# Kernel optimization log

Hardware: AMD Instinct MI355X
Metric: run time of the kernel (lower is better)

## Reference

```python
import jax, jax.numpy as jnp
from jax import lax
import numpy as np

B, COND_C = 16, 256
IN_C, OUT_C, K = 64, 64, 3
H = W = 128
N_PARAM = K * K * IN_C * OUT_C + OUT_C  # 36928


def setup_inputs() -> dict:
    key = jax.random.key(0)
    k1, k2, k3, k4 = jax.random.split(key, 4)
    x = jax.random.normal(k1, (B, IN_C, H, W), dtype=jnp.float32)
    conditioning = jax.random.normal(k2, (B, COND_C), dtype=jnp.float32)
    # nn.Linear(cond_c, n_param): weight [n_param, cond_c], bias [n_param]
    W_cond = jax.random.normal(k3, (N_PARAM, COND_C), dtype=jnp.float32) * 0.02
    b_cond = jax.random.normal(k4, (N_PARAM,), dtype=jnp.float32) * 0.02
    return {"x": x, "conditioning": conditioning, "W_cond": W_cond, "b_cond": b_cond}


def reference(x, conditioning, W_cond, b_cond):
    # Hypernetwork: Linear + tanh*5 (ConditionerActivation)
    w_b = jnp.tanh(conditioning @ W_cond.T + b_cond) * 5.0  # [B, N_PARAM]
    bias = w_b[:, -OUT_C:]                                   # [B, out_c]
    w = w_b[:, :-OUT_C].reshape(B, OUT_C, IN_C, K, K)        # per-sample OIHW

    def conv_one(xi, wi, bi):
        # xi: [in_c, H, W], wi: [out_c, in_c, K, K], bi: [out_c]
        y = lax.conv_general_dilated(
            xi[None], wi,
            window_strides=(1, 1),
            padding=[(1, 1), (1, 1)],
            dimension_numbers=("NCHW", "OIHW", "NCHW"),
        )[0]
        return y + bi[:, None, None]

    return jax.vmap(conv_one)(x, w, bias)  # [B, out_c, H, W]
```

## Files before the change

### kernel.cpp

```cpp
#include <hip/hip_runtime.h>
#include <math.h>
#include <stdint.h>

#define B_    16
#define CONDC 256
#define ICn   64
#define OCn   64
#define Hn    128
#define Wn    128
#define NW    36864
#define NPARAM 36928

typedef _Float16 half8 __attribute__((ext_vector_type(8)));
typedef _Float16 half4 __attribute__((ext_vector_type(4)));
typedef float f32x4 __attribute__((ext_vector_type(4)));
typedef float f32x16 __attribute__((ext_vector_type(16)));

__device__ inline unsigned pk2(float a, float b) {
    union { _Float16 h[2]; unsigned u; } q;
    q.h[0] = (_Float16)a; q.h[1] = (_Float16)b;
    return q.u;
}

__global__ void transpose_k(const float* __restrict__ x, _Float16* __restrict__ xt) {
    __shared__ unsigned ls[4160];
    const int tid = threadIdx.x;
    const int bx  = blockIdx.x;

    if (bx < 2048) {
        const int b = bx >> 7, y = bx & 127;
        const float* xrow = x + (size_t)b * 1048576 + (size_t)y * 128;

        float4 va[4], vb[4];
        #pragma unroll
        for (int t = 0; t < 4; ++t) {
            int u = t * 256 + tid;
            int icp = u >> 5, xg = u & 31;
            const float* r0 = xrow + (size_t)(2 * icp) * 16384;
            va[t] = *((const float4*)r0 + xg);
            vb[t] = *((const float4*)(r0 + 16384) + xg);
        }
        __builtin_amdgcn_sched_barrier(0);

        #pragma unroll
        for (int t = 0; t < 4; ++t) {
            int u = t * 256 + tid;
            int icp = u >> 5, xg = u & 31;
            unsigned* dst = ls + icp * 130 + 4 * xg;
            *(uint2*)(dst)     = make_uint2(pk2(va[t].x, vb[t].x), pk2(va[t].y, vb[t].y));
            *(uint2*)(dst + 2) = make_uint2(pk2(va[t].z, vb[t].z), pk2(va[t].w, vb[t].w));
        }
        __syncthreads();

        _Float16* rowhalf = xt + (size_t)(b * 130 + y + 1) * 8320;
        #pragma unroll
        for (int t = 0; t < 5; ++t) {
            int u = t * 256 + tid;
            if (u < 1040) {
                int xp = u >> 3, g = u & 7;
                uint4 val = make_uint4(0u, 0u, 0u, 0u);
                if (xp > 0 && xp < 129) {
                    int xx = xp - 1;
                    val.x = ls[(4 * g + 0) * 130 + xx];
                    val.y = ls[(4 * g + 1) * 130 + xx];
                    val.z = ls[(4 * g + 2) * 130 + xx];
                    val.w = ls[(4 * g + 3) * 130 + xx];
                }
                *(uint4*)(rowhalf + (size_t)u * 8) = val;
            }
        }
    } else {
        const int q = bx - 2048;
        const int b = q >> 1, yp = (q & 1) ? 129 : 0;
        _Float16* rowhalf = xt + (size_t)(b * 130 + yp) * 8320;
        uint4 z = make_uint4(0u, 0u, 0u, 0u);
        for (int u = tid; u < 1040; u += 256)
            *(uint4*)(rowhalf + (size_t)u * 8) = z;
    }
}

__global__ __launch_bounds__(256, 4) void gemm_k(const float* __restrict__ cond,
                                                 const float* __restrict__ Wc,
                                                 const float* __restrict__ bc,
                                                 _Float16* __restrict__ wt,
                                                 float* __restrict__ bias) {
    __shared__ _Float16 wl[64 * 280];
    const int tid = threadIdx.x;
    const int pbase = blockIdx.x * 64;

    float4 v[16];
    #pragma unroll
    for (int t = 0; t < 16; ++t) {
        int u = t * 256 + tid;
        int pl = u >> 6, kg = u & 63;
        v[t] = *((const float4*)(Wc + (size_t)(pbase + pl) * 256) + kg);
    }
    __builtin_amdgcn_sched_barrier(0);

    #pragma unroll
    for (int t = 0; t < 16; ++t) {
        int u = t * 256 + tid;
        int pl = u >> 6, kg = u & 63;
        half4 h = { (_Float16)v[t].x, (_Float16)v[t].y, (_Float16)v[t].z, (_Float16)v[t].w };
        *(half4*)(wl + pl * 280 + kg * 4) = h;
    }
    __syncthreads();

    const int w = tid >> 6, l = tid & 63, n = l & 15, r4 = l >> 4;
    const _Float16* arow = wl + (w * 16 + n) * 280 + r4 * 8;
    const float*    crow = cond + n * 256 + r4 * 8;
    f32x4 acc = (f32x4){0.f, 0.f, 0.f, 0.f};
    #pragma unroll
    for (int kk = 0; kk < 8; ++kk) {
        half8 av = *(const half8*)(arow + kk * 32);
        float4 u0 = *(const float4*)(crow + kk * 32);
        float4 u1 = *(const float4*)(crow + kk * 32 + 4);
        half8 bv;
        bv[0] = (_Float16)u0.x; bv[1] = (_Float16)u0.y; bv[2] = (_Float16)u0.z; bv[3] = (_Float16)u0.w;
        bv[4] = (_Float16)u1.x; bv[5] = (_Float16)u1.y; bv[6] = (_Float16)u1.z; bv[7] = (_Float16)u1.w;
        acc = __builtin_amdgcn_mfma_f32_16x16x32_f16(av, bv, acc, 0, 0, 0);
    }
    #pragma unroll
    for (int j = 0; j < 4; ++j) {
        int p = pbase + w * 16 + r4 * 4 + j;
        float vv = tanhf(acc[j] + bc[p]) * 5.0f;
        if (p < NW) {
            int oc = p / 576, rem = p - oc * 576;
            int ic = rem / 9,  t  = rem - ic * 9;
            int icq = ic >> 4, icl = ic & 15;
            wt[((((size_t)n * 4 + icq) * 9 + t) * 64 + oc) * 16 + icl] = (_Float16)vv;
        } else {
            bias[n * 64 + (p - NW)] = vv;
        }
    }
}

__global__ __launch_bounds__(256, 4) void conv_v7(const _Float16* __restrict__ xt,
                                                  const _Float16* __restrict__ wt,
                                                  const float* __restrict__ bias,
                                                  float* __restrict__ out) {
    __shared__ _Float16 xs[3 * 6144];
    const int tid = threadIdx.x;
    const int l   = tid & 63;
    const int w   = tid >> 6;
    const int px  = l & 31;
    const int jj  = l >> 5;
    const int ot  = w & 1;
    const int rg  = w >> 1;

    const int sw = (blockIdx.x & 7) * 128 + (blockIdx.x >> 3);
    const int Xt = sw & 3, Yt = (sw >> 2) & 15, b = sw >> 6;
    const int X0  = Xt * 32;
    const int Y0g = Yt * 8;

    const _Float16* xbase = xt + ((size_t)(b * 130 + Y0g) * 130 + X0) * 64;
    const _Float16* wbat  = wt + (size_t)b * 36864 + (size_t)(ot * 32 + px) * 16 + jj * 8;

    int offkw[3];
    #pragma unroll
    for (int kw = 0; kw < 3; ++kw) {
        int c = (px + kw) * 2 + jj;
        offkw[kw] = (c ^ ((c >> 3) & 7)) * 16;
    }
    const int Lb = rg * 4;

    #define STAGEQ(ICQ, BUF) do {                                                       \
        _Pragma("unroll")                                                               \
        for (int it = 0; it < 3; ++it) {                                                \
            int d   = it * 256 + tid;                                                   \
            int row = (int)((unsigned)d / 72u);                                         \
            int c   = d - row * 72;                                                     \
            int cs  = c ^ ((c >> 3) & 7);                                               \
            const _Float16* src = xbase + (size_t)row * 8320 + (cs >> 1) * 64           \
                                + (ICQ) * 16 + (cs & 1) * 8;                            \
            __builtin_amdgcn_global_load_lds(                                           \
                (const __attribute__((address_space(1))) void*)src,                     \
                (__attribute__((address_space(3))) void*)((__attribute__((address_space(3))) char*)xs + (BUF) * 12288 + (it * 256 + (tid & ~63)) * 16), \
                16, 0, 0);                                                              \
        } } while (0)

    #define COMPUTE(ICQ, BUF) do {                                                      \
        const char* bufb = (const char*)xs + (BUF) * 12288;                             \
        const _Float16* wq = wbat + (size_t)(ICQ) * 9216;                               \
        _Pragma("unroll")                                                               \
        for (int kw = 0; kw < 3; ++kw) {                                                \
            half8 Bf[6];                                                                \
            _Pragma("unroll")                                                           \
            for (int iy = 0; iy < 6; ++iy)                                              \
                Bf[iy] = *(const half8*)(bufb + (Lb + iy) * 1152 + offkw[kw]);          \
            _Pragma("unroll")                                                           \
            for (int iy = 0; iy < 6; ++iy) {                                            \
                _Pragma("unroll")                                                       \
                for (int kh = 0; kh < 3; ++kh) {                                        \
                    const int r = iy - kh;                                              \
                    if (r >= 0 && r < 4)                                                \
                        acc[r] = __builtin_amdgcn_mfma_f32_32x32x16_f16(                \
                            *(const half8*)(wq + (kh * 3 + kw) * 1024), Bf[iy], acc[r], 0, 0, 0); \
                } } } } while (0)

    f32x16 acc[4];
    #pragma unroll
    for (int r = 0; r < 4; ++r) acc[r] = (f32x16){};

    STAGEQ(0, 0); STAGEQ(1, 1); STAGEQ(2, 2);
    __builtin_amdgcn_sched_barrier(0);

    asm volatile("s_waitcnt vmcnt(6)" ::: "memory");
    __builtin_amdgcn_sched_barrier(0);
    __builtin_amdgcn_s_barrier();
    __builtin_amdgcn_sched_barrier(0);
    COMPUTE(0, 0);
    asm volatile("s_waitcnt lgkmcnt(0)" ::: "memory");
    __builtin_amdgcn_sched_barrier(0);
    __builtin_amdgcn_s_barrier();
    __builtin_amdgcn_sched_barrier(0);
    STAGEQ(3, 0);
    __builtin_amdgcn_sched_barrier(0);

    asm volatile("s_waitcnt vmcnt(6)" ::: "memory");
    __builtin_amdgcn_sched_barrier(0);
    __builtin_amdgcn_s_barrier();
    __builtin_amdgcn_sched_barrier(0);
    COMPUTE(1, 1);

    asm volatile("s_waitcnt vmcnt(3)" ::: "memory");
    __builtin_amdgcn_sched_barrier(0);
    __builtin_amdgcn_s_barrier();
    __builtin_amdgcn_sched_barrier(0);
    COMPUTE(2, 2);

    asm volatile("s_waitcnt vmcnt(0)" ::: "memory");
    __builtin_amdgcn_sched_barrier(0);
    __builtin_amdgcn_s_barrier();
    __builtin_amdgcn_sched_barrier(0);
    COMPUTE(3, 0);

    #undef STAGEQ
    #undef COMPUTE

    const float* bb = bias + b * 64;
    #pragma unroll
    for (int r = 0; r < 4; ++r) {
        const int yo = Y0g + Lb + r;
        float* ob = out + (((size_t)(b * 64 + ot * 32)) * 128 + yo) * 128 + X0 + px;
        #pragma unroll
        for (int reg = 0; reg < 16; ++reg) {
            const int ocl = (reg & 3) + 8 * (reg >> 2) + 4 * jj;
            ob[(size_t)ocl * 16384] = acc[r][reg] + bb[ot * 32 + ocl];
        }
    }
}

__global__ __launch_bounds__(256) void cond_gemm(const float* __restrict__ cond,
                                                 const float* __restrict__ Wc,
                                                 const float* __restrict__ bc,
                                                 float* __restrict__ wb) {
    __shared__ float condl[B_][CONDC + 1];
    __shared__ float Wl[16][CONDC + 1];
    const int tid = threadIdx.x;
    const int p0 = blockIdx.x * 16;
    for (int i = tid; i < B_ * CONDC; i += 256) condl[i >> 8][i & 255] = cond[i];
    for (int i = tid; i < 16 * CONDC; i += 256) {
        int pl = i >> 8, k = i & 255;
        Wl[pl][k] = Wc[(p0 + pl) * CONDC + k];
    }
    __syncthreads();
    const int pl = tid >> 4;
    const int b  = tid & 15;
    float acc = bc[p0 + pl];
    #pragma unroll 8
    for (int k = 0; k < CONDC; ++k) acc += Wl[pl][k] * condl[b][k];
    wb[b * NPARAM + p0 + pl] = tanhf(acc) * 5.0f;
}

#define TS  32
#define OG  8
#define ICC 8
__global__ __launch_bounds__(256) void conv_kernel(const float* __restrict__ x,
                                                   const float* __restrict__ wb,
                                                   float* __restrict__ out) {
    __shared__ float fxs[ICC][TS + 2][TS + 2];
    __shared__ float ws[OG][ICC][9];
    const int tid = threadIdx.x;
    const int b   = blockIdx.z;
    const int ocg = blockIdx.y * OG;
    const int tx0 = (blockIdx.x & 3) * TS;
    const int ty0 = (blockIdx.x >> 2) * TS;
    const int px  = (tid & 15) * 2;
    const int py  = (tid >> 4) * 2;
    float acc[OG][4];
    #pragma unroll
    for (int o = 0; o < OG; ++o)
        #pragma unroll
        for (int q = 0; q < 4; ++q) acc[o][q] = 0.0f;
    const float* wbase = wb + b * NPARAM;
    for (int ic0 = 0; ic0 < ICn; ic0 += ICC) {
        for (int i = tid; i < ICC * (TS + 2) * (TS + 2); i += 256) {
            int icl = i / ((TS + 2) * (TS + 2));
            int rem = i % ((TS + 2) * (TS + 2));
            int yy = rem / (TS + 2), xx = rem % (TS + 2);
            int gy = ty0 - 1 + yy, gx = tx0 - 1 + xx;
            float v = 0.0f;
            if (gy >= 0 && gy < Hn && gx >= 0 && gx < Wn)
                v = x[((b * ICn + ic0 + icl) * Hn + gy) * Wn + gx];
            fxs[icl][yy][xx] = v;
        }
        for (int i = tid; i < OG * ICC * 9; i += 256) {
            int o = i / (ICC * 9), rem = i % (ICC * 9);
            int icl = rem / 9, k = rem % 9;
            ws[o][icl][k] = wbase[((ocg + o) * ICn + ic0 + icl) * 9 + k];
        }
        __syncthreads();
        #pragma unroll
        for (int icl = 0; icl < ICC; ++icl) {
            float xv[4][4];
            #pragma unroll
            for (int dy = 0; dy < 4; ++dy)
                #pragma unroll
                for (int dx = 0; dx < 4; ++dx) xv[dy][dx] = fxs[icl][py + dy][px + dx];
            #pragma unroll
            for (int o = 0; o < OG; ++o)
                #pragma unroll
                for (int kh = 0; kh < 3; ++kh)
                    #pragma unroll
                    for (int kw = 0; kw < 3; ++kw) {
                        float wv = ws[o][icl][kh * 3 + kw];
                        acc[o][0] += xv[kh][kw] * wv;
                        acc[o][1] += xv[kh][kw + 1] * wv;
                        acc[o][2] += xv[kh + 1][kw] * wv;
                        acc[o][3] += xv[kh + 1][kw + 1] * wv;
                    }
        }
        __syncthreads();
    }
    #pragma unroll
    for (int o = 0; o < OG; ++o) {
        float bias = wbase[NW + ocg + o];
        int oc = ocg + o;
        float* obase = out + ((size_t)(b * OCn + oc) * Hn + (ty0 + py)) * Wn + tx0 + px;
        obase[0] = acc[o][0] + bias;
        obase[1] = acc[o][1] + bias;
        obase[Wn] = acc[o][2] + bias;
        obase[Wn + 1] = acc[o][3] + bias;
    }
}

extern "C" void kernel_launch(void* const* d_in, const int* in_sizes, int n_in,
                              void* d_out, int out_size, void* d_ws, size_t ws_size,
                              hipStream_t stream) {
    const float* x    = (const float*)d_in[0];
    const float* cond = (const float*)d_in[1];
    const float* Wc   = (const float*)d_in[2];
    const float* bc   = (const float*)d_in[3];
    float* out = (float*)d_out;

    const size_t WT_BYTES = (size_t)B_ * 9 * 64 * 64 * 2;
    const size_t BIAS_OFF = WT_BYTES;
    const size_t XT_OFF   = 1183744;
    const size_t XT_BYTES = (size_t)B_ * 130 * 130 * 64 * 2 + 32768;
    const size_t NEED     = XT_OFF + XT_BYTES;

    if (ws_size >= NEED) {
        _Float16* wt   = (_Float16*)d_ws;
        float*    bias = (float*)((char*)d_ws + BIAS_OFF);
        _Float16* xt   = (_Float16*)((char*)d_ws + XT_OFF);
        transpose_k<<<dim3(2048 + 32), 256, 0, stream>>>(x, xt);
        gemm_k<<<dim3(577), 256, 0, stream>>>(cond, Wc, bc, wt, bias);
        conv_v7<<<dim3(1024), 256, 0, stream>>>(xt, wt, bias, out);
    } else {
        float* wbuf = (float*)d_ws;
        cond_gemm<<<dim3(NPARAM / 16), 256, 0, stream>>>(cond, Wc, bc, wbuf);
        conv_kernel<<<dim3(16, OCn / OG, B_), 256, 0, stream>>>(x, wbuf, out);
    }
}
```

Baseline: 65.07 us.

## Use direct global-to-LDS loads with XOR swizzle in transpose and hypernet GEMM

The transpose and hypernetwork GEMM kernels now load tiles straight from global memory into LDS with global_load_lds instead of staging them through registers. The FP32 data stays in LDS with an XOR-swizzled layout, and the fp16 conversion happens when the data is read back. The GEMM switches to 32-parameter tiles with 128 threads and twice as many blocks. This is meant to cut register pressure and VGPR-to-LDS store instructions, at the cost of more LDS traffic (FP32 instead of packed half) and extra conversion work on the read side.

```diff
diff --git a/kernel.cpp b/kernel.cpp
--- a/kernel.cpp
+++ b/kernel.cpp
@@ -22,8 +22,15 @@
     return q.u;
 }
 
+#define GLOAD_LDS(SRC, LDSOFF)                                                          \
+    __builtin_amdgcn_global_load_lds(                                                   \
+        (const __attribute__((address_space(1))) void*)(SRC),                           \
+        (__attribute__((address_space(3))) void*)((__attribute__((address_space(3))) char*)lds_base + (LDSOFF)), \
+        16, 0, 0)
+
 __global__ void transpose_k(const float* __restrict__ x, _Float16* __restrict__ xt) {
-    __shared__ unsigned ls[4160];
+    __shared__ float ls[8192];
+    char* lds_base = (char*)ls;
     const int tid = threadIdx.x;
     const int bx  = blockIdx.x;
 
@@ -31,26 +38,18 @@
         const int b = bx >> 7, y = bx & 127;
         const float* xrow = x + (size_t)b * 1048576 + (size_t)y * 128;
 
-        float4 va[4], vb[4];
-        #pragma unroll
-        for (int t = 0; t < 4; ++t) {
-            int u = t * 256 + tid;
-            int icp = u >> 5, xg = u & 31;
-            const float* r0 = xrow + (size_t)(2 * icp) * 16384;
-            va[t] = *((const float4*)r0 + xg);
-            vb[t] = *((const float4*)(r0 + 16384) + xg);
-        }
+        #pragma unroll
+        for (int it = 0; it < 8; ++it) {
+            int d   = it * 256 + tid;
+            int ic  = d >> 5, xcd = d & 31;
+            int xc  = xcd ^ (ic & 7) ^ ((ic >> 3) & 7);
+            const float* src = xrow + (size_t)ic * 16384 + xc * 4;
+            GLOAD_LDS(src, (it * 256 + (tid & ~63)) * 16);
+        }
+        asm volatile("s_waitcnt vmcnt(0)" ::: "memory");
         __builtin_amdgcn_sched_barrier(0);
-
-        #pragma unroll
-        for (int t = 0; t < 4; ++t) {
-            int u = t * 256 + tid;
-            int icp = u >> 5, xg = u & 31;
-            unsigned* dst = ls + icp * 130 + 4 * xg;
-            *(uint2*)(dst)     = make_uint2(pk2(va[t].x, vb[t].x), pk2(va[t].y, vb[t].y));
-            *(uint2*)(dst + 2) = make_uint2(pk2(va[t].z, vb[t].z), pk2(va[t].w, vb[t].w));
-        }
-        __syncthreads();
+        __builtin_amdgcn_s_barrier();
+        __builtin_amdgcn_sched_barrier(0);
 
         _Float16* rowhalf = xt + (size_t)(b * 130 + y + 1) * 8320;
         #pragma unroll
@@ -61,10 +60,17 @@
                 uint4 val = make_uint4(0u, 0u, 0u, 0u);
                 if (xp > 0 && xp < 129) {
                     int xx = xp - 1;
-                    val.x = ls[(4 * g + 0) * 130 + xx];
-                    val.y = ls[(4 * g + 1) * 130 + xx];
-                    val.z = ls[(4 * g + 2) * 130 + xx];
-                    val.w = ls[(4 * g + 3) * 130 + xx];
+                    int cb = (xx >> 2), eo = (xx & 3);
+                    float f[8];
+                    #pragma unroll
+                    for (int j = 0; j < 8; ++j) {
+                        int ic = 8 * g + j;
+                        f[j] = ls[ic * 128 + ((cb ^ (ic & 7) ^ ((ic >> 3) & 7)) << 2) + eo];
+                    }
+                    val.x = pk2(f[0], f[1]);
+                    val.y = pk2(f[2], f[3]);
+                    val.z = pk2(f[4], f[5]);
+                    val.w = pk2(f[6], f[7]);
                 }
                 *(uint4*)(rowhalf + (size_t)u * 8) = val;
             }
@@ -79,40 +85,42 @@
     }
 }
 
-__global__ __launch_bounds__(256, 4) void gemm_k(const float* __restrict__ cond,
-                                                 const float* __restrict__ Wc,
-                                                 const float* __restrict__ bc,
-                                                 _Float16* __restrict__ wt,
-                                                 float* __restrict__ bias) {
-    __shared__ _Float16 wl[64 * 280];
-    const int tid = threadIdx.x;
-    const int pbase = blockIdx.x * 64;
-
-    float4 v[16];
-    #pragma unroll
-    for (int t = 0; t < 16; ++t) {
-        int u = t * 256 + tid;
-        int pl = u >> 6, kg = u & 63;
-        v[t] = *((const float4*)(Wc + (size_t)(pbase + pl) * 256) + kg);
-    }
-    __builtin_amdgcn_sched_barrier(0);
-
-    #pragma unroll
-    for (int t = 0; t < 16; ++t) {
-        int u = t * 256 + tid;
-        int pl = u >> 6, kg = u & 63;
-        half4 h = { (_Float16)v[t].x, (_Float16)v[t].y, (_Float16)v[t].z, (_Float16)v[t].w };
-        *(half4*)(wl + pl * 280 + kg * 4) = h;
-    }
-    __syncthreads();
+__global__ void gemm_k(const float* __restrict__ cond,
+                       const float* __restrict__ Wc,
+                       const float* __restrict__ bc,
+                       _Float16* __restrict__ wt,
+                       float* __restrict__ bias) {
+    __shared__ float wl[8192];
+    char* lds_base = (char*)wl;
+    const int tid = threadIdx.x;
+    const int pbase = blockIdx.x * 32;
+
+    #pragma unroll
+    for (int it = 0; it < 16; ++it) {
+        int d   = it * 128 + tid;
+        int pl  = d >> 6, kgd = d & 63;
+        int kg  = kgd ^ (pl & 7);
+        const float* src = Wc + (size_t)(pbase + pl) * 256 + kg * 4;
+        GLOAD_LDS(src, (it * 128 + (tid & ~63)) * 16);
+    }
+    asm volatile("s_waitcnt vmcnt(0)" ::: "memory");
+    __builtin_amdgcn_sched_barrier(0);
+    __builtin_amdgcn_s_barrier();
+    __builtin_amdgcn_sched_barrier(0);
 
     const int w = tid >> 6, l = tid & 63, n = l & 15, r4 = l >> 4;
-    const _Float16* arow = wl + (w * 16 + n) * 280 + r4 * 8;
-    const float*    crow = cond + n * 256 + r4 * 8;
+    const int pl = w * 16 + n;
+    const float* crow = cond + n * 256 + r4 * 8;
+
     f32x4 acc = (f32x4){0.f, 0.f, 0.f, 0.f};
     #pragma unroll
     for (int kk = 0; kk < 8; ++kk) {
-        half8 av = *(const half8*)(arow + kk * 32);
+        const int c0 = kk * 8 + r4 * 2;
+        float4 a0 = *(const float4*)((const char*)wl + pl * 1024 + ((c0 ^ (pl & 7)) << 4));
+        float4 a1 = *(const float4*)((const char*)wl + pl * 1024 + (((c0 + 1) ^ (pl & 7)) << 4));
+        half8 av;
+        av[0] = (_Float16)a0.x; av[1] = (_Float16)a0.y; av[2] = (_Float16)a0.z; av[3] = (_Float16)a0.w;
+        av[4] = (_Float16)a1.x; av[5] = (_Float16)a1.y; av[6] = (_Float16)a1.z; av[7] = (_Float16)a1.w;
         float4 u0 = *(const float4*)(crow + kk * 32);
         float4 u1 = *(const float4*)(crow + kk * 32 + 4);
         half8 bv;
@@ -365,7 +373,7 @@
         float*    bias = (float*)((char*)d_ws + BIAS_OFF);
         _Float16* xt   = (_Float16*)((char*)d_ws + XT_OFF);
         transpose_k<<<dim3(2048 + 32), 256, 0, stream>>>(x, xt);
-        gemm_k<<<dim3(577), 256, 0, stream>>>(cond, Wc, bc, wt, bias);
+        gemm_k<<<dim3(1154), 128, 0, stream>>>(cond, Wc, bc, wt, bias);
         conv_v7<<<dim3(1024), 256, 0, stream>>>(xt, wt, bias, out);
     } else {
         float* wbuf = (float*)d_ws;
```

Measured after the change: 66.41 us. 1.02x slower.
